# Kernel optimization log

Hardware: AMD Instinct MI355X
Metric: run time of the kernel (lower is better)

Reference implementation:

```python
import jax, jax.numpy as jnp
import numpy as np

D = 2048      # hidden_size
W = 4         # kernel_size
DG = 2048     # generator hidden size (no reduction)

def setup_inputs() -> dict:
    key = jax.random.key(0)
    k1, k2, k3, k4 = jax.random.split(key, 4)
    x = jax.random.normal(k1, (2, 4096, D), dtype=jnp.float32)
    # Linear weights stored torch-style [out, in]; scaled small for sane activations
    w1 = jax.random.normal(k2, (DG, D), dtype=jnp.float32) * 0.02
    w2 = jax.random.normal(k3, (D * W, DG), dtype=jnp.float32) * 0.02
    b2 = jax.random.normal(k4, (D * W,), dtype=jnp.float32) * 0.02
    return {"x": x, "w1": w1, "w2": w2, "b2": b2}

def reference(x, w1, w2, b2):
    B, T, Dh = x.shape
    # kernel generator: w2(silu(w1 @ x)) + b2 -> per-position kernels [B,T,D,W]
    h = jax.nn.silu(jnp.einsum('btd,gd->btg', x, w1))
    flat = jnp.einsum('btg,kg->btk', h, w2) + b2
    kernels = flat.reshape(B, T, Dh, W)
    # causal depthwise dynamic conv: y[b,t,d] = sum_w x[b, t-(W-1)+w, d] * k[b,t,d,w]
    xp = jnp.pad(x, ((0, 0), (W - 1, 0), (0, 0)))
    y = xp[:, 0:T, :] * kernels[..., 0]
    for w in range(1, W):  # small fixed-width loop over kernel taps
        y = y + xp[:, w:w + T, :] * kernels[..., w]
    return jax.nn.silu(y)
```

## Files before the change

kernel.cpp:

```cpp
#include <hip/hip_runtime.h>
#include <cstdint>

#define D_DIM  2048
#define T_DIM  4096
#define B_DIM  2
#define M_DIM  8192
#define DG_DIM 2048
#define N2_DIM 8192
#define K_DIM  2048
#define NT_TILES (K_DIM / 64)

typedef __bf16 bf16x8 __attribute__((ext_vector_type(8)));
typedef __bf16 bf16x4 __attribute__((ext_vector_type(4)));
typedef float  f32x4  __attribute__((ext_vector_type(4)));

__device__ __forceinline__ void gload_lds16(const void* g, void* l) {
  __builtin_amdgcn_global_load_lds(
      (__attribute__((address_space(1))) void*)g,
      (__attribute__((address_space(3))) void*)l, 16, 0, 0);
}

__device__ __forceinline__ float silu_f(float a) {
  return a / (1.f + __expf(-a));
}

__global__ void cast_f32_bf16(const float* __restrict__ src,
                              __bf16* __restrict__ dst, int n4) {
  int i = blockIdx.x * blockDim.x + threadIdx.x;
  if (i >= n4) return;
  float4 v = ((const float4*)src)[i];
  bf16x4 o;
  o[0] = (__bf16)v.x; o[1] = (__bf16)v.y; o[2] = (__bf16)v.z; o[3] = (__bf16)v.w;
  ((bf16x4*)dst)[i] = o;
}

__global__ void cast_permute_w2(const float* __restrict__ src,
                                __bf16* __restrict__ dst, int n4) {
  int i = blockIdx.x * blockDim.x + threadIdx.x;
  if (i >= n4) return;
  const int row = i >> 9;
  const int pos = i & 511;
  const int blk = row >> 8;
  const int cw  = row & 255;
  const int j   = cw >> 6;
  const int wn  = (cw >> 4) & 3;
  const int ln  = cw & 15;
  const int d   = blk * 64 + wn * 16 + ln;
  const int k   = 4 * d + j;
  float4 v = ((const float4*)src)[(size_t)k * 512 + pos];
  bf16x4 o;
  o[0] = (__bf16)v.x; o[1] = (__bf16)v.y; o[2] = (__bf16)v.z; o[3] = (__bf16)v.w;
  ((bf16x4*)dst)[i] = o;
}


__device__ __forceinline__ void stage_unit(const __bf16* src0, const __bf16* src1,
                                           __bf16* sX, int s, int hf,
                                           int lq0, int lq1) {
  const int k0 = (s < NT_TILES) ? (s * 64) : 0;
  __bf16* dst = sX + ((s & 1) * 2 + hf) * 8192;
  const size_t goff = (size_t)hf * 128 * K_DIM + k0;
  gload_lds16(src0 + goff, dst + lq0);
  gload_lds16(src1 + goff, dst + lq1);
}

__device__ __forceinline__ void read4(bf16x8 dst[4][2], const __bf16* base,
                                      const int off[4][2]) {
#pragma unroll
  for (int i = 0; i < 4; i++) {
    dst[i][0] = *(const bf16x8*)(base + off[i][0]);
    dst[i][1] = *(const bf16x8*)(base + off[i][1]);
  }
}

__device__ __forceinline__ void read2(bf16x8 dst[2][2], const __bf16* base,
                                      const int off[2][2]) {
#pragma unroll
  for (int j = 0; j < 2; j++) {
    dst[j][0] = *(const bf16x8*)(base + off[j][0]);
    dst[j][1] = *(const bf16x8*)(base + off[j][1]);
  }
}

__device__ __forceinline__ void mmaq(f32x4 acc[8][4], int ib, int jb,
                                     const bf16x8 a[4][2], const bf16x8 b[2][2]) {
#pragma unroll
  for (int kk = 0; kk < 2; kk++)
#pragma unroll
    for (int i = 0; i < 4; i++)
#pragma unroll
      for (int j = 0; j < 2; j++)
        acc[ib + i][jb + j] = __builtin_amdgcn_mfma_f32_16x16x32_bf16(
            a[i][kk], b[j][kk], acc[ib + i][jb + j], 0, 0, 0);
}

__device__ __forceinline__ void phase_mid() {
  __builtin_amdgcn_s_barrier();
  asm volatile("s_waitcnt lgkmcnt(0)" ::: "memory");
  __builtin_amdgcn_sched_barrier(0);
  __builtin_amdgcn_s_setprio(1);
}

__device__ __forceinline__ void phase_end() {
  __builtin_amdgcn_s_setprio(0);
  __builtin_amdgcn_s_barrier();
}

__device__ __forceinline__ void gemm_core(const __bf16* __restrict__ A,
                                          const __bf16* __restrict__ B,
                                          int m0, int n0,
                                          __bf16* sA, __bf16* sB,
                                          f32x4 acc[8][4]) {
  constexpr int K = K_DIM;
  const int t    = threadIdx.x;
  const int lane = t & 63;
  const int wv   = t >> 6;
  const int wm   = wv >> 2;
  const int wn   = wv & 3;
  const int ln   = lane & 15, qd = lane >> 4;

  const __bf16 *a_src0, *a_src1, *b_src0, *b_src1;
  int lq0, lq1;
  {
    int q = t, row = q >> 3, cg = (q & 7) ^ (row & 7);
    a_src0 = A + (size_t)(m0 + row) * K + cg * 8;
    b_src0 = B + (size_t)(n0 + row) * K + cg * 8;
    lq0 = q * 8;
    q = 512 + t; row = q >> 3; cg = (q & 7) ^ (row & 7);
    a_src1 = A + (size_t)(m0 + row) * K + cg * 8;
    b_src1 = B + (size_t)(n0 + row) * K + cg * 8;
    lq1 = q * 8;
  }

  int aoff[4][2], boff[2][2];
#pragma unroll
  for (int i = 0; i < 4; i++)
#pragma unroll
    for (int kk = 0; kk < 2; kk++) {
      const int row = wm * 16 + i * 32 + ln;
      aoff[i][kk] = row * 64 + (((kk * 4 + qd) ^ (row & 7)) << 3);
    }
#pragma unroll
  for (int j = 0; j < 2; j++)
#pragma unroll
    for (int kk = 0; kk < 2; kk++) {
      const int row = j * 64 + wn * 16 + ln;
      boff[j][kk] = row * 64 + (((kk * 4 + qd) ^ (row & 7)) << 3);
    }

  bf16x8 aL[4][2], aH[4][2], b0[2][2], b1[2][2];

  stage_unit(a_src0, a_src1, sA, 0, 0, lq0, lq1);
  stage_unit(b_src0, b_src1, sB, 0, 0, lq0, lq1);
  stage_unit(a_src0, a_src1, sA, 0, 1, lq0, lq1);
  stage_unit(b_src0, b_src1, sB, 0, 1, lq0, lq1);
  stage_unit(a_src0, a_src1, sA, 1, 0, lq0, lq1);
  stage_unit(b_src0, b_src1, sB, 1, 0, lq0, lq1);
  stage_unit(a_src0, a_src1, sA, 1, 1, lq0, lq1);
  asm volatile("s_waitcnt vmcnt(6)" ::: "memory");
  __builtin_amdgcn_s_barrier();

  for (int t0 = 0; t0 < NT_TILES; ++t0) {
    const int p = t0 & 1;
    const __bf16* A0h = sA + p * 16384;
    const __bf16* B0h = sB + p * 16384;

    read4(aL, A0h, aoff);
    read2(b0, B0h, boff);
    stage_unit(b_src0, b_src1, sB, t0 + 1, 1, lq0, lq1);
    phase_mid();
    mmaq(acc, 0, 0, aL, b0);
    phase_end();

    read4(aH, A0h + 8192, aoff);
    stage_unit(a_src0, a_src1, sA, t0 + 2, 0, lq0, lq1);
    phase_mid();
    mmaq(acc, 4, 0, aH, b0);
    phase_end();

    read2(b1, B0h + 8192, boff);
    stage_unit(b_src0, b_src1, sB, t0 + 2, 0, lq0, lq1);
    phase_mid();
    mmaq(acc, 0, 2, aL, b1);
    phase_end();

    stage_unit(a_src0, a_src1, sA, t0 + 2, 1, lq0, lq1);
    asm volatile("s_waitcnt vmcnt(6)" ::: "memory");
    __builtin_amdgcn_s_barrier();
    __builtin_amdgcn_s_setprio(1);
    mmaq(acc, 4, 2, aH, b1);
    __builtin_amdgcn_s_setprio(0);
    __builtin_amdgcn_s_barrier();
  }
  asm volatile("s_waitcnt vmcnt(0)" ::: "memory");
}

__global__ __launch_bounds__(512) void gemm1_silu(
    const __bf16* __restrict__ A, const __bf16* __restrict__ B,
    __bf16* __restrict__ H) {
  __shared__ __bf16 sA[4 * 8192];
  __shared__ __bf16 sB[4 * 8192];
  const int m0 = blockIdx.y * 256, n0 = blockIdx.x * 256;
  f32x4 acc[8][4] = {};
  gemm_core(A, B, m0, n0, sA, sB, acc);

  const int lane = threadIdx.x & 63;
  const int wv   = threadIdx.x >> 6;
  const int wm   = wv >> 2, wn = wv & 3;
  const int ln   = lane & 15, qd = lane >> 4;
#pragma unroll
  for (int i = 0; i < 8; i++) {
    const int row0 = m0 + wm * 16 + i * 32 + qd * 4;
#pragma unroll
    for (int j = 0; j < 4; j++) {
      const int col = n0 + wn * 16 + j * 64 + ln;
#pragma unroll
      for (int r = 0; r < 4; r++)
        H[(size_t)(row0 + r) * DG_DIM + col] = (__bf16)silu_f(acc[i][j][r]);
    }
  }
}

__global__ __launch_bounds__(512) void gemm2_conv_silu(
    const __bf16* __restrict__ A, const __bf16* __restrict__ B,
    const float* __restrict__ b2, const float* __restrict__ x,
    float* __restrict__ out) {
  __shared__ __bf16 sA[4 * 8192];
  __shared__ __bf16 sB[4 * 8192];
  const int m0 = blockIdx.y * 256, n0 = blockIdx.x * 256;
  f32x4 acc[8][4] = {};
  gemm_core(A, B, m0, n0, sA, sB, acc);

  const int lane = threadIdx.x & 63;
  const int wv   = threadIdx.x >> 6;
  const int wm   = wv >> 2, wn = wv & 3;
  const int ln   = lane & 15, qd = lane >> 4;

  const int d = (n0 >> 2) + wn * 16 + ln;
  const float4 bias = *(const float4*)(b2 + 4 * d);

#pragma unroll
  for (int i = 0; i < 8; i++) {
    const int m_base = m0 + wm * 16 + i * 32 + qd * 4;
    const int b  = m_base >> 12;
    const int tb = m_base & 4095;
    float xv[7];
#pragma unroll
    for (int s = 0; s < 7; s++) {
      const int tp = tb + s - 3;
      xv[s] = (tp >= 0) ? x[((size_t)((b << 12) + tp)) * D_DIM + d] : 0.f;
    }
#pragma unroll
    for (int r = 0; r < 4; r++) {
      float y = (acc[i][0][r] + bias.x) * xv[r + 0]
              + (acc[i][1][r] + bias.y) * xv[r + 1]
              + (acc[i][2][r] + bias.z) * xv[r + 2]
              + (acc[i][3][r] + bias.w) * xv[r + 3];
      out[(size_t)(m_base + r) * D_DIM + d] = silu_f(y);
    }
  }
}

extern "C" void kernel_launch(void* const* d_in, const int* in_sizes, int n_in,
                              void* d_out, int out_size, void* d_ws, size_t ws_size,
                              hipStream_t stream) {
  (void)in_sizes; (void)n_in; (void)out_size; (void)ws_size;
  const float* x  = (const float*)d_in[0];
  const float* w1 = (const float*)d_in[1];
  const float* w2 = (const float*)d_in[2];
  const float* b2 = (const float*)d_in[3];
  float* out = (float*)d_out;

  __bf16* xb  = (__bf16*)d_ws;
  __bf16* w1b = xb  + (size_t)M_DIM * D_DIM;
  __bf16* w2b = w1b + (size_t)DG_DIM * D_DIM;
  __bf16* hb  = w2b + (size_t)N2_DIM * DG_DIM;

  {
    int n4 = M_DIM * D_DIM / 4;
    cast_f32_bf16<<<(n4 + 255) / 256, 256, 0, stream>>>(x, xb, n4);
  }
  {
    int n4 = DG_DIM * D_DIM / 4;
    cast_f32_bf16<<<(n4 + 255) / 256, 256, 0, stream>>>(w1, w1b, n4);
  }
  {
    int n4 = N2_DIM * DG_DIM / 4;
    cast_permute_w2<<<(n4 + 255) / 256, 256, 0, stream>>>(w2, w2b, n4);
  }

  gemm1_silu<<<dim3(DG_DIM / 256, M_DIM / 256), 512, 0, stream>>>(xb, w1b, hb);
  gemm2_conv_silu<<<dim3(N2_DIM / 256, M_DIM / 256), 512, 0, stream>>>(
      hb, w2b, b2, x, out);
}
```

Before: 498.3 us.

## Restructure GEMM main loop: bulk fragment reads, then barrier-free MFMA phases

The four-phase loop that interleaved LDS fragment reads, barriers and MFMA quadrants is replaced. Each iteration now issues all global-to-LDS stages between the four MFMA quadrants with no barriers in between, then reads every A/B fragment for the next tile in one block behind two barriers. The loop is unrolled by two with fixed ping-pong buffer pointers, and the second-source address is computed as an offset instead of kept in extra registers. The aim is fewer barriers and less scheduling overhead per K-tile, at the cost of holding all fragments in registers at once and losing overlap between LDS reads and MFMAs.

```diff
diff --git a/kernel.cpp b/kernel.cpp
--- a/kernel.cpp
+++ b/kernel.cpp
@@ -54,14 +54,13 @@
 }
 
 
-__device__ __forceinline__ void stage_unit(const __bf16* src0, const __bf16* src1,
-                                           __bf16* sX, int s, int hf,
-                                           int lq0, int lq1) {
+__device__ __forceinline__ void stage_unit(const __bf16* src, __bf16* sX,
+                                           int s, int hf, int lq0) {
   const int k0 = (s < NT_TILES) ? (s * 64) : 0;
   __bf16* dst = sX + ((s & 1) * 2 + hf) * 8192;
   const size_t goff = (size_t)hf * 128 * K_DIM + k0;
-  gload_lds16(src0 + goff, dst + lq0);
-  gload_lds16(src1 + goff, dst + lq1);
+  gload_lds16(src + goff, dst + lq0);
+  gload_lds16(src + goff + (size_t)64 * K_DIM, dst + lq0 + 4096);
 }
 
 __device__ __forceinline__ void read4(bf16x8 dst[4][2], const __bf16* base,
@@ -84,6 +83,7 @@
 
 __device__ __forceinline__ void mmaq(f32x4 acc[8][4], int ib, int jb,
                                      const bf16x8 a[4][2], const bf16x8 b[2][2]) {
+  __builtin_amdgcn_s_setprio(1);
 #pragma unroll
   for (int kk = 0; kk < 2; kk++)
 #pragma unroll
@@ -92,18 +92,7 @@
       for (int j = 0; j < 2; j++)
         acc[ib + i][jb + j] = __builtin_amdgcn_mfma_f32_16x16x32_bf16(
             a[i][kk], b[j][kk], acc[ib + i][jb + j], 0, 0, 0);
-}
-
-__device__ __forceinline__ void phase_mid() {
-  __builtin_amdgcn_s_barrier();
-  asm volatile("s_waitcnt lgkmcnt(0)" ::: "memory");
-  __builtin_amdgcn_sched_barrier(0);
-  __builtin_amdgcn_s_setprio(1);
-}
-
-__device__ __forceinline__ void phase_end() {
   __builtin_amdgcn_s_setprio(0);
-  __builtin_amdgcn_s_barrier();
 }
 
 __device__ __forceinline__ void gemm_core(const __bf16* __restrict__ A,
@@ -119,17 +108,13 @@
   const int wn   = wv & 3;
   const int ln   = lane & 15, qd = lane >> 4;
 
-  const __bf16 *a_src0, *a_src1, *b_src0, *b_src1;
-  int lq0, lq1;
+  const __bf16 *a_src, *b_src;
+  int lq0;
   {
     int q = t, row = q >> 3, cg = (q & 7) ^ (row & 7);
-    a_src0 = A + (size_t)(m0 + row) * K + cg * 8;
-    b_src0 = B + (size_t)(n0 + row) * K + cg * 8;
+    a_src = A + (size_t)(m0 + row) * K + cg * 8;
+    b_src = B + (size_t)(n0 + row) * K + cg * 8;
     lq0 = q * 8;
-    q = 512 + t; row = q >> 3; cg = (q & 7) ^ (row & 7);
-    a_src1 = A + (size_t)(m0 + row) * K + cg * 8;
-    b_src1 = B + (size_t)(n0 + row) * K + cg * 8;
-    lq1 = q * 8;
   }
 
   int aoff[4][2], boff[2][2];
@@ -148,49 +133,75 @@
       boff[j][kk] = row * 64 + (((kk * 4 + qd) ^ (row & 7)) << 3);
     }
 
+  const __bf16* A_p0 = sA;           const __bf16* A_p1 = sA + 16384;
+  const __bf16* B_p0 = sB;           const __bf16* B_p1 = sB + 16384;
+
   bf16x8 aL[4][2], aH[4][2], b0[2][2], b1[2][2];
 
-  stage_unit(a_src0, a_src1, sA, 0, 0, lq0, lq1);
-  stage_unit(b_src0, b_src1, sB, 0, 0, lq0, lq1);
-  stage_unit(a_src0, a_src1, sA, 0, 1, lq0, lq1);
-  stage_unit(b_src0, b_src1, sB, 0, 1, lq0, lq1);
-  stage_unit(a_src0, a_src1, sA, 1, 0, lq0, lq1);
-  stage_unit(b_src0, b_src1, sB, 1, 0, lq0, lq1);
-  stage_unit(a_src0, a_src1, sA, 1, 1, lq0, lq1);
+  stage_unit(a_src, sA, 0, 0, lq0);
+  stage_unit(b_src, sB, 0, 0, lq0);
+  stage_unit(a_src, sA, 0, 1, lq0);
+  stage_unit(b_src, sB, 0, 1, lq0);
+  stage_unit(a_src, sA, 1, 0, lq0);
+  stage_unit(b_src, sB, 1, 0, lq0);
+  stage_unit(a_src, sA, 1, 1, lq0);
   asm volatile("s_waitcnt vmcnt(6)" ::: "memory");
   __builtin_amdgcn_s_barrier();
-
-  for (int t0 = 0; t0 < NT_TILES; ++t0) {
-    const int p = t0 & 1;
-    const __bf16* A0h = sA + p * 16384;
-    const __bf16* B0h = sB + p * 16384;
-
-    read4(aL, A0h, aoff);
-    read2(b0, B0h, boff);
-    stage_unit(b_src0, b_src1, sB, t0 + 1, 1, lq0, lq1);
-    phase_mid();
-    mmaq(acc, 0, 0, aL, b0);
-    phase_end();
-
-    read4(aH, A0h + 8192, aoff);
-    stage_unit(a_src0, a_src1, sA, t0 + 2, 0, lq0, lq1);
-    phase_mid();
-    mmaq(acc, 4, 0, aH, b0);
-    phase_end();
-
-    read2(b1, B0h + 8192, boff);
-    stage_unit(b_src0, b_src1, sB, t0 + 2, 0, lq0, lq1);
-    phase_mid();
-    mmaq(acc, 0, 2, aL, b1);
-    phase_end();
-
-    stage_unit(a_src0, a_src1, sA, t0 + 2, 1, lq0, lq1);
-    asm volatile("s_waitcnt vmcnt(6)" ::: "memory");
-    __builtin_amdgcn_s_barrier();
-    __builtin_amdgcn_s_setprio(1);
-    mmaq(acc, 4, 2, aH, b1);
-    __builtin_amdgcn_s_setprio(0);
-    __builtin_amdgcn_s_barrier();
+  __builtin_amdgcn_sched_barrier(0);
+  read4(aL, A_p0, aoff);
+  read4(aH, A_p0 + 8192, aoff);
+  read2(b0, B_p0, boff);
+  read2(b1, B_p0 + 8192, boff);
+  asm volatile("s_waitcnt lgkmcnt(0)" ::: "memory");
+  __builtin_amdgcn_sched_barrier(0);
+  __builtin_amdgcn_s_barrier();
+  __builtin_amdgcn_sched_barrier(0);
+
+  for (int it = 0; it < NT_TILES / 2; ++it) {
+    {
+      const int s1 = 2 * it + 1, s2 = 2 * it + 2;
+      stage_unit(b_src, sB, s1, 1, lq0);
+      mmaq(acc, 0, 0, aL, b0);
+      stage_unit(a_src, sA, s2, 0, lq0);
+      mmaq(acc, 4, 0, aH, b0);
+      stage_unit(b_src, sB, s2, 0, lq0);
+      mmaq(acc, 0, 2, aL, b1);
+      stage_unit(a_src, sA, s2, 1, lq0);
+      mmaq(acc, 4, 2, aH, b1);
+      asm volatile("s_waitcnt vmcnt(6)" ::: "memory");
+      __builtin_amdgcn_s_barrier();
+      __builtin_amdgcn_sched_barrier(0);
+      read4(aL, A_p1, aoff);
+      read4(aH, A_p1 + 8192, aoff);
+      read2(b0, B_p1, boff);
+      read2(b1, B_p1 + 8192, boff);
+      asm volatile("s_waitcnt lgkmcnt(0)" ::: "memory");
+      __builtin_amdgcn_sched_barrier(0);
+      __builtin_amdgcn_s_barrier();
+      __builtin_amdgcn_sched_barrier(0);
+    }
+    {
+      const int s1 = 2 * it + 2, s2 = 2 * it + 3;
+      stage_unit(b_src, sB, s1, 1, lq0);
+      mmaq(acc, 0, 0, aL, b0);
+      stage_unit(a_src, sA, s2, 0, lq0);
+      mmaq(acc, 4, 0, aH, b0);
+      stage_unit(b_src, sB, s2, 0, lq0);
+      mmaq(acc, 0, 2, aL, b1);
+      stage_unit(a_src, sA, s2, 1, lq0);
+      mmaq(acc, 4, 2, aH, b1);
+      asm volatile("s_waitcnt vmcnt(6)" ::: "memory");
+      __builtin_amdgcn_s_barrier();
+      __builtin_amdgcn_sched_barrier(0);
+      read4(aL, A_p0, aoff);
+      read4(aH, A_p0 + 8192, aoff);
+      read2(b0, B_p0, boff);
+      read2(b1, B_p0 + 8192, boff);
+      asm volatile("s_waitcnt lgkmcnt(0)" ::: "memory");
+      __builtin_amdgcn_sched_barrier(0);
+      __builtin_amdgcn_s_barrier();
+      __builtin_amdgcn_sched_barrier(0);
+    }
   }
   asm volatile("s_waitcnt vmcnt(0)" ::: "memory");
 }
```

After: 476.4 us. 4.4% less time.
